# Performance work log

Hardware: AMD Instinct MI355X
Metric: run time of the kernel (lower is better)

The kernel has to match this reference:

```python
import jax, jax.numpy as jnp
import numpy as np

PSEUDO3D = True
DO_TUBE = True
DILATION_ITERATIONS = 1

# Neighbor offsets P2..P9 (clockwise from north), as in Zhang-Suen / skimage skeletonize
_OFFS = [(-1, 0), (-1, 1), (0, 1), (1, 1), (1, 0), (1, -1), (0, -1), (-1, -1)]


def _shift(a, dy, dx):
    # out[n, y, x] = a[n, y+dy, x+dx], zero-padded borders (same as skimage's 0-pad)
    N, H, W = a.shape
    p = jnp.pad(a, ((0, 0), (1, 1), (1, 1)))
    return p[:, 1 + dy:1 + dy + H, 1 + dx:1 + dx + W]


def _subiter(img, first):
    # One Zhang-Suen sub-iteration on a stack of 2D slices [N, H, W] (bool)
    P = [_shift(img, dy, dx) for dy, dx in _OFFS]
    B = sum(p.astype(jnp.int32) for p in P)            # nonzero-neighbor count
    seq = P + [P[0]]
    A = sum(((~seq[k]) & seq[k + 1]).astype(jnp.int32) for k in range(8))  # 0->1 transitions
    P2, P3, P4, P5, P6, P7, P8, P9 = P
    if first:
        c = (~(P2 & P4 & P6)) & (~(P4 & P6 & P8))
    else:
        c = (~(P2 & P4 & P8)) & (~(P2 & P6 & P8))
    remove = img & (B >= 2) & (B <= 6) & (A == 1) & c
    return img & ~remove


def _thin_stack(stack):
    # Zhang-Suen thinning of every 2D slice in a [N, H, W] bool stack, run to convergence.
    # All slices are processed in one while_loop; converged slices are fixed points, so
    # extra iterations are no-ops and the result matches per-slice skeletonize.
    def body(state):
        img, _ = state
        new = _subiter(_subiter(img, True), False)
        return new, jnp.any(new != img)

    def cond(state):
        return state[1]

    img, _ = jax.lax.while_loop(cond, body, (stack, jnp.array(True)))
    return img


def _dilate6(v):
    # scipy.ndimage.binary_dilation with the default 6-connected 3D structure, border 0
    D, H, W = v.shape
    p = jnp.pad(v, 1)
    out = v
    for dz, dy, dx in [(1, 0, 0), (-1, 0, 0), (0, 1, 0), (0, -1, 0), (0, 0, 1), (0, 0, -1)]:
        out = out | p[1 + dz:1 + dz + D, 1 + dy:1 + dy + H, 1 + dx:1 + dx + W]
    return out


def setup_inputs() -> dict:
    key = jax.random.key(0)
    gt = jax.random.randint(key, (1, 48, 384, 384), 0, 2).astype(jnp.float32)
    return {"gt_skel": gt}


def reference(gt_skel):
    vol = gt_skel[0]                      # squeeze(axis=0) -> [D, H, W]
    mask = vol == 1.0                     # bool
    skel = _thin_stack(mask)              # per z-slice skeletonize
    if PSEUDO3D:
        # per y-slice: mask[:, y, :] has shape [D, W]
        skel = skel | jnp.transpose(_thin_stack(jnp.transpose(mask, (1, 0, 2))), (1, 0, 2))
        # per x-slice: mask[:, :, x] has shape [D, H]
        skel = skel | jnp.transpose(_thin_stack(jnp.transpose(mask, (2, 0, 1))), (1, 2, 0))
    if DO_TUBE:
        for _ in range(DILATION_ITERATIONS):
            skel = _dilate6(skel)
    skel = skel & mask                    # skel &= gt_skel.astype(bool) (values are 0/1)
    return skel[None].astype(jnp.float32)
```

## Files before the change

### kernel.cpp

```cpp
#include <hip/hip_runtime.h>

typedef unsigned long long u64;

constexpr int D = 48, H = 384, W = 384;
constexpr int WPR = 6;
constexpr int PADW = 8;
constexpr int NVOX = D * H * W;
constexpr int NWVOL = D * H * WPR;
constexpr int MPAD2 = 52;

__device__ __forceinline__ void fa(u64 a, u64 b, u64 c, u64& s, u64& cy) {
  u64 x = a ^ b;
  s = x ^ c;
  cy = (a & b) | (c & x);
}

__device__ __forceinline__ u64 zs_regs(u64 w00, u64 w01, u64 w02,
                                       u64 w10, u64 w11, u64 w12,
                                       u64 w20, u64 w21, u64 w22, bool first) {
  const u64 P2 = w01;
  const u64 P3 = (w01 >> 1) | (w02 << 63);
  const u64 P4 = (w11 >> 1) | (w12 << 63);
  const u64 P5 = (w21 >> 1) | (w22 << 63);
  const u64 P6 = w21;
  const u64 P7 = (w21 << 1) | (w20 >> 63);
  const u64 P8 = (w11 << 1) | (w10 >> 63);
  const u64 P9 = (w01 << 1) | (w00 >> 63);

  u64 s1, c1, s2, c2, s3, c3, u0, u1, v1, v2;
  fa(P2, P3, P4, s1, c1);
  fa(P5, P6, P7, s2, c2);
  fa(P8, P9, 0ull, s3, c3);
  fa(s1, s2, s3, u0, u1);
  fa(c1, c2, c3, v1, v2);
  u64 b1 = u1 ^ v1, k2 = u1 & v1;
  u64 b2 = v2 ^ k2, b3 = v2 & k2;
  u64 condB = (b1 | b2 | b3) & ~(b3 | (b2 & b1 & u0));

  u64 t0 = ~P2 & P3, t1 = ~P3 & P4, t2 = ~P4 & P5, t3 = ~P5 & P6;
  u64 t4 = ~P6 & P7, t5 = ~P7 & P8, t6 = ~P8 & P9, t7 = ~P9 & P2;
  fa(t0, t1, t2, s1, c1);
  fa(t3, t4, t5, s2, c2);
  fa(t6, t7, 0ull, s3, c3);
  fa(s1, s2, s3, u0, u1);
  fa(c1, c2, c3, v1, v2);
  u64 a1 = u1 ^ v1, j2 = u1 & v1;
  u64 a2 = v2 ^ j2, a3 = v2 & j2;
  u64 condA = u0 & ~(a1 | a2 | a3);

  u64 cc = first ? ((~(P2 & P4 & P6)) & (~(P4 & P6 & P8)))
                 : ((~(P2 & P4 & P8)) & (~(P2 & P6 & P8)));
  return w11 & ~(condB & condA & cc);
}

__device__ __forceinline__ bool dirty3(const u64* U, int q) {
  const int pb = q + 64;
  const int w = pb >> 6, sh = pb & 63;
  u64 v = U[w] >> sh;
  if (sh > 61) v |= U[w + 1] << (64 - sh);
  return (v & 7ull) != 0;
}

template<int R, bool FIRST>
__device__ __forceinline__ void subpass(const u64* __restrict__ src, u64* __restrict__ dst,
                                        u64* rawW, const u64* rawPrev,
                                        u64* Uw, const u64* Ur,
                                        int* chgflag, int tid, int nthr) {
  constexpr int NP = (R + 2) * PADW;
  int anych = 0;
  for (int base = 0; base < NP; base += nthr) {
    const int idx = base + tid;
    int changed = 0;
    if (idx < NP) {
      const bool dirty = dirty3(Ur, idx - PADW - 1)
                       | dirty3(Ur, idx - 1)
                       | dirty3(Ur, idx + PADW - 1);
      if (dirty) {
        const u64 old = src[idx];
        u64 nw = 0;
        if (old) {
          const u64 n00 = src[idx - PADW - 1];
          const u64 n01 = src[idx - PADW];
          const u64 n02 = src[idx - PADW + 1];
          const u64 n10 = src[idx - 1];
          const u64 n12 = src[idx + 1];
          const u64 n20 = src[idx + PADW - 1];
          const u64 n21 = src[idx + PADW];
          const u64 n22 = src[idx + PADW + 1];
          nw = zs_regs(n00, n01, n02, n10, old, n12, n20, n21, n22, FIRST);
          changed = (nw != old);
        }
        dst[idx] = nw;
        anych |= changed;
      }
    }
    const u64 bal = __ballot(changed != 0);
    if ((tid & 63) == 0 && idx < NP) {
      const int mw = 1 + (idx >> 6);
      rawW[mw] = bal;
      Uw[mw] = bal | rawPrev[mw];
    }
  }
  if (anych) *chgflag = 1;
}

template<int R, int MODE>
__device__ __forceinline__ void thin_body(const u64* __restrict__ maskP,
                                          u64* __restrict__ skelZY,
                                          u64* __restrict__ skelX,
                                          int slice, u64* Abuf, u64* Bbuf,
                                          u64 (*raw)[MPAD2], u64 (*Um)[MPAD2],
                                          int* s_chg) {
  constexpr int NP = (R + 2) * PADW;
  constexpr int MW = (NP + 63) >> 6;
  const int tid = threadIdx.x;
  const int nthr = blockDim.x;

  if (MODE == 0 || MODE == 1) {
    for (int idx = tid; idx < NP; idx += nthr) {
      const int rp = idx >> 3, cp = idx & 7;
      u64 v = 0;
      if (rp >= 1 && rp <= R && cp >= 1 && cp <= 6) {
        if (MODE == 0) v = maskP[(slice * H + (rp - 1)) * WPR + (cp - 1)];
        else           v = maskP[((rp - 1) * H + slice) * WPR + (cp - 1)];
      }
      Abuf[idx] = v;
      Bbuf[idx] = 0;
    }
  } else {
    const int lane = tid & 63, wave = tid >> 6, nwv = nthr >> 6;
    const int xw = slice >> 6, xb = slice & 63;
    for (int w = wave; w < NP; w += nwv) {
      const int rp = w >> 3, cp = w & 7;
      u64 val = 0;
      if (rp >= 1 && rp <= R && cp >= 1 && cp <= 6) {
        const int c = (cp - 1) * 64 + lane;
        u64 bit = (maskP[((rp - 1) * H + c) * WPR + xw] >> xb) & 1ull;
        val = __ballot(bit != 0);
      }
      if (lane == 0) { Abuf[w] = val; Bbuf[w] = 0; }
    }
  }

  for (int t = tid; t < 4 * MPAD2; t += nthr) {
    const int arr = t / MPAD2, j = t - arr * MPAD2;
    const u64 v = ((arr & 1) && j >= 1 && j <= MW) ? ~0ull : 0ull;
    if (arr < 2) raw[arr][j] = v; else Um[arr - 2][j] = v;
  }
  if (tid < 2) s_chg[tid] = 0;
  __syncthreads();

  int k = 0;
  while (true) {
    subpass<R, true >(Abuf, Bbuf, raw[0], raw[1], Um[0], Um[1], &s_chg[k], tid, nthr);
    __syncthreads();
    if (tid == 0) s_chg[k ^ 1] = 0;
    subpass<R, false>(Bbuf, Abuf, raw[1], raw[0], Um[1], Um[0], &s_chg[k], tid, nthr);
    __syncthreads();
    if (s_chg[k] == 0) break;
    k ^= 1;
  }

  for (int idx = tid; idx < NP; idx += nthr) {
    const int rp = idx >> 3, cp = idx & 7;
    if (rp < 1 || rp > R || cp < 1 || cp > 6) continue;
    const u64 w = Abuf[idx];
    if (!w) continue;
    const int r = rp - 1, wc = cp - 1;
    if (MODE == 0)      atomicOr(&skelZY[(slice * H + r) * WPR + wc], w);
    else if (MODE == 1) atomicOr(&skelZY[(r * H + slice) * WPR + wc], w);
    else                skelX[(r * W + slice) * WPR + wc] = w;
  }
}

__global__ __launch_bounds__(1024) void thin_all(const u64* __restrict__ maskP,
                                                 u64* __restrict__ skelZY,
                                                 u64* __restrict__ skelX) {
  __shared__ u64 Abuf[(H + 2) * PADW];
  __shared__ u64 Bbuf[(H + 2) * PADW];
  __shared__ u64 raw[2][MPAD2];
  __shared__ u64 Um[2][MPAD2];
  __shared__ int s_chg[2];
  const int b = blockIdx.x;
  if (b < D) {
    thin_body<H, 0>(maskP, skelZY, skelX, b, Abuf, Bbuf, raw, Um, s_chg);
  } else if (b < D + H) {
    thin_body<D, 1>(maskP, skelZY, skelX, b - D, Abuf, Bbuf, raw, Um, s_chg);
  } else {
    thin_body<D, 2>(maskP, skelZY, skelX, b - D - H, Abuf, Bbuf, raw, Um, s_chg);
  }
}

__global__ void init_pack(const float* __restrict__ in, u64* __restrict__ maskP,
                          u64* __restrict__ skelZY, u64* __restrict__ skelX) {
  const int lane = threadIdx.x & 63;
  const int gwave = (blockIdx.x * blockDim.x + threadIdx.x) >> 6;
  const int nwaves = (gridDim.x * blockDim.x) >> 6;
  for (int widx = gwave; widx < NWVOL; widx += nwaves) {
    float v = in[(size_t)widx * 64 + lane];
    u64 w = __ballot(v == 1.0f);
    if (lane == 0) {
      maskP[widx] = w;
      skelZY[widx] = 0;
      skelX[widx] = 0;
    }
  }
}

__global__ void transpose_or(const u64* __restrict__ skelX,
                             u64* __restrict__ skelZY) {
  const int gw = (blockIdx.x * blockDim.x + threadIdx.x) >> 6;
  const int lane = threadIdx.x & 63;
  const int z = gw / 36, rem = gw - z * 36;
  const int yw = rem / 6, xw = rem - yw * 6;
  const int x = xw * 64 + lane;
  const u64 wx = skelX[(z * W + x) * WPR + yw];
  u64 mine = 0;
  #pragma unroll 8
  for (int j = 0; j < 64; ++j) {
    u64 wj = __ballot((wx >> j) & 1ull);
    if (lane == j) mine = wj;
  }
  const int y = yw * 64 + lane;
  if (mine) skelZY[(z * H + y) * WPR + xw] |= mine;
}

__global__ __launch_bounds__(256) void dilate_expand(const u64* __restrict__ maskP,
                                                     const u64* __restrict__ skelZY,
                                                     float* __restrict__ out) {
  __shared__ u64 rw[64];
  const int tid = threadIdx.x;
  const int wbase = blockIdx.x * 64;
  if (tid < 64) {
    const int wi = wbase + tid;
    const int wc = wi % WPR;
    const int row = wi / WPR;
    const int y = row % H;
    const int z = row / H;
    const u64 S = skelZY[wi];
    const u64 L = (wc > 0) ? skelZY[wi - 1] : 0ull;
    const u64 Rw = (wc < WPR - 1) ? skelZY[wi + 1] : 0ull;
    u64 d = S | (S << 1) | (L >> 63) | (S >> 1) | (Rw << 63);
    if (y > 0)     d |= skelZY[wi - WPR];
    if (y < H - 1) d |= skelZY[wi + WPR];
    if (z > 0)     d |= skelZY[wi - H * WPR];
    if (z < D - 1) d |= skelZY[wi + H * WPR];
    rw[tid] = d & maskP[wi];
  }
  __syncthreads();
  float4* o4 = reinterpret_cast<float4*>(out + (size_t)wbase * 64);
  #pragma unroll
  for (int k = 0; k < 4; ++k) {
    const int f = tid + 256 * k;
    const u64 bits = rw[f >> 4] >> ((f & 15) * 4);
    float4 o;
    o.x = (float)(bits & 1ull);
    o.y = (float)((bits >> 1) & 1ull);
    o.z = (float)((bits >> 2) & 1ull);
    o.w = (float)((bits >> 3) & 1ull);
    o4[f] = o;
  }
}

extern "C" void kernel_launch(void* const* d_in, const int* in_sizes, int n_in,
                              void* d_out, int out_size, void* d_ws, size_t ws_size,
                              hipStream_t stream) {
  const float* in = (const float*)d_in[0];
  float* out = (float*)d_out;
  u64* wsw = (u64*)d_ws;
  u64* maskP = wsw;
  u64* skelZY = wsw + NWVOL;
  u64* skelX = wsw + 2 * NWVOL;

  init_pack<<<1728, 256, 0, stream>>>(in, maskP, skelZY, skelX);
  thin_all<<<D + H + W, 1024, 0, stream>>>(maskP, skelZY, skelX);
  transpose_or<<<(NWVOL + 255) / 256, 256, 0, stream>>>(skelX, skelZY);
  dilate_expand<<<NWVOL / 64, 256, 0, stream>>>(maskP, skelZY, out);
}
```

Baseline: 70.70 us.

## Split z-slice thinning into haloed band pre-pass, then finish per full slice

The 48 long z-slice thinning blocks (384 rows each) were the critical path in a single launch. They are now split into 4 bands per slice with 24-row halos, each run for a fixed number of Zhang-Suen iterations alongside the x/y-slice blocks. A second kernel then finishes convergence on the full slices starting from that partial result, and fuses the x-skeleton transpose-OR using atomics. This adds redundant halo work, one more workspace buffer, and relies on the band result being a valid intermediate state so the finish pass converges to the same skeleton.

```diff
diff --git a/kernel.cpp b/kernel.cpp
--- a/kernel.cpp
+++ b/kernel.cpp
@@ -8,6 +8,13 @@
 constexpr int NVOX = D * H * W;
 constexpr int NWVOL = D * H * WPR;
 constexpr int MPAD2 = 52;
+
+constexpr int BAND = 96;
+constexpr int HALO = 24;
+constexpr int KA = 24;
+constexpr int BROWS = BAND + 2 * HALO;
+constexpr int NBAND = H / BAND;
+constexpr int NTILE = D * 36;
 
 __device__ __forceinline__ void fa(u64 a, u64 b, u64 c, u64& s, u64& cy) {
   u64 x = a ^ b;
@@ -79,15 +86,9 @@
         const u64 old = src[idx];
         u64 nw = 0;
         if (old) {
-          const u64 n00 = src[idx - PADW - 1];
-          const u64 n01 = src[idx - PADW];
-          const u64 n02 = src[idx - PADW + 1];
-          const u64 n10 = src[idx - 1];
-          const u64 n12 = src[idx + 1];
-          const u64 n20 = src[idx + PADW - 1];
-          const u64 n21 = src[idx + PADW];
-          const u64 n22 = src[idx + PADW + 1];
-          nw = zs_regs(n00, n01, n02, n10, old, n12, n20, n21, n22, FIRST);
+          nw = zs_regs(src[idx - PADW - 1], src[idx - PADW], src[idx - PADW + 1],
+                       src[idx - 1], old, src[idx + 1],
+                       src[idx + PADW - 1], src[idx + PADW], src[idx + PADW + 1], FIRST);
           changed = (nw != old);
         }
         dst[idx] = nw;
@@ -104,8 +105,17 @@
   if (anych) *chgflag = 1;
 }
 
+__device__ __forceinline__ void init_masks(u64 (*raw)[MPAD2], u64 (*Um)[MPAD2],
+                                           int MW, int tid, int nthr) {
+  for (int t = tid; t < 4 * MPAD2; t += nthr) {
+    const int arr = t / MPAD2, j = t - arr * MPAD2;
+    const u64 v = ((arr & 1) && j >= 1 && j <= MW) ? ~0ull : 0ull;
+    if (arr < 2) raw[arr][j] = v; else Um[arr - 2][j] = v;
+  }
+}
+
 template<int R, int MODE>
-__device__ __forceinline__ void thin_body(const u64* __restrict__ maskP,
+__device__ __forceinline__ void thin_body(const u64* __restrict__ src0,
                                           u64* __restrict__ skelZY,
                                           u64* __restrict__ skelX,
                                           int slice, u64* Abuf, u64* Bbuf,
@@ -121,8 +131,8 @@
       const int rp = idx >> 3, cp = idx & 7;
       u64 v = 0;
       if (rp >= 1 && rp <= R && cp >= 1 && cp <= 6) {
-        if (MODE == 0) v = maskP[(slice * H + (rp - 1)) * WPR + (cp - 1)];
-        else           v = maskP[((rp - 1) * H + slice) * WPR + (cp - 1)];
+        if (MODE == 0) v = src0[(slice * H + (rp - 1)) * WPR + (cp - 1)];
+        else           v = src0[((rp - 1) * H + slice) * WPR + (cp - 1)];
       }
       Abuf[idx] = v;
       Bbuf[idx] = 0;
@@ -135,18 +145,14 @@
       u64 val = 0;
       if (rp >= 1 && rp <= R && cp >= 1 && cp <= 6) {
         const int c = (cp - 1) * 64 + lane;
-        u64 bit = (maskP[((rp - 1) * H + c) * WPR + xw] >> xb) & 1ull;
+        u64 bit = (src0[((rp - 1) * H + c) * WPR + xw] >> xb) & 1ull;
         val = __ballot(bit != 0);
       }
       if (lane == 0) { Abuf[w] = val; Bbuf[w] = 0; }
     }
   }
 
-  for (int t = tid; t < 4 * MPAD2; t += nthr) {
-    const int arr = t / MPAD2, j = t - arr * MPAD2;
-    const u64 v = ((arr & 1) && j >= 1 && j <= MW) ? ~0ull : 0ull;
-    if (arr < 2) raw[arr][j] = v; else Um[arr - 2][j] = v;
-  }
+  init_masks(raw, Um, MW, tid, nthr);
   if (tid < 2) s_chg[tid] = 0;
   __syncthreads();
 
@@ -173,9 +179,69 @@
   }
 }
 
-__global__ __launch_bounds__(1024) void thin_all(const u64* __restrict__ maskP,
-                                                 u64* __restrict__ skelZY,
-                                                 u64* __restrict__ skelX) {
+__device__ __forceinline__ void band_body(const u64* __restrict__ maskP,
+                                          u64* __restrict__ curZ,
+                                          int zi, int band,
+                                          u64* Abuf, u64* Bbuf,
+                                          u64 (*raw)[MPAD2], u64 (*Um)[MPAD2],
+                                          int* s_chg) {
+  constexpr int NP = (BROWS + 2) * PADW;
+  constexpr int MW = (NP + 63) >> 6;
+  const int tid = threadIdx.x;
+  const int nthr = blockDim.x;
+  const int g0 = band * BAND - HALO;
+
+  for (int idx = tid; idx < NP; idx += nthr) {
+    const int rp = idx >> 3, cp = idx & 7;
+    const int g = g0 + rp - 1;
+    u64 v = 0;
+    if (rp >= 1 && rp <= BROWS && cp >= 1 && cp <= 6 && g >= 0 && g < H)
+      v = maskP[(zi * H + g) * WPR + (cp - 1)];
+    Abuf[idx] = v;
+    Bbuf[idx] = 0;
+  }
+  init_masks(raw, Um, MW, tid, nthr);
+  if (tid == 0) s_chg[0] = 0;
+  __syncthreads();
+
+  for (int t = 0; t < KA; t += 2) {
+    subpass<BROWS, true >(Abuf, Bbuf, raw[0], raw[1], Um[0], Um[1], &s_chg[0], tid, nthr);
+    __syncthreads();
+    subpass<BROWS, false>(Bbuf, Abuf, raw[1], raw[0], Um[1], Um[0], &s_chg[0], tid, nthr);
+    __syncthreads();
+  }
+
+  for (int idx = tid; idx < NP; idx += nthr) {
+    const int rp = idx >> 3, cp = idx & 7;
+    if (rp < 1 || rp > BROWS || cp < 1 || cp > 6) continue;
+    const int g = g0 + rp - 1;
+    if (g < band * BAND || g >= band * BAND + BAND) continue;
+    curZ[(zi * H + g) * WPR + (cp - 1)] = Abuf[idx];
+  }
+}
+
+__global__ __launch_bounds__(1024) void thin_bands_xy(const u64* __restrict__ maskP,
+                                                      u64* __restrict__ skelZY,
+                                                      u64* __restrict__ skelX,
+                                                      u64* __restrict__ curZ) {
+  __shared__ u64 Abuf[(BROWS + 2) * PADW];
+  __shared__ u64 Bbuf[(BROWS + 2) * PADW];
+  __shared__ u64 raw[2][MPAD2];
+  __shared__ u64 Um[2][MPAD2];
+  __shared__ int s_chg[2];
+  const int b = blockIdx.x;
+  if (b < D * NBAND) {
+    band_body(maskP, curZ, b >> 2, b & 3, Abuf, Bbuf, raw, Um, s_chg);
+  } else if (b < D * NBAND + W) {
+    thin_body<D, 2>(maskP, skelZY, skelX, b - D * NBAND, Abuf, Bbuf, raw, Um, s_chg);
+  } else {
+    thin_body<D, 1>(maskP, skelZY, skelX, b - D * NBAND - W, Abuf, Bbuf, raw, Um, s_chg);
+  }
+}
+
+__global__ __launch_bounds__(1024) void thin_z_finish(const u64* __restrict__ curZ,
+                                                      u64* __restrict__ skelZY,
+                                                      const u64* __restrict__ skelX) {
   __shared__ u64 Abuf[(H + 2) * PADW];
   __shared__ u64 Bbuf[(H + 2) * PADW];
   __shared__ u64 raw[2][MPAD2];
@@ -183,11 +249,24 @@
   __shared__ int s_chg[2];
   const int b = blockIdx.x;
   if (b < D) {
-    thin_body<H, 0>(maskP, skelZY, skelX, b, Abuf, Bbuf, raw, Um, s_chg);
-  } else if (b < D + H) {
-    thin_body<D, 1>(maskP, skelZY, skelX, b - D, Abuf, Bbuf, raw, Um, s_chg);
+    thin_body<H, 0>(curZ, skelZY, nullptr, b, Abuf, Bbuf, raw, Um, s_chg);
   } else {
-    thin_body<D, 2>(maskP, skelZY, skelX, b - D - H, Abuf, Bbuf, raw, Um, s_chg);
+    const int gw = (b - D) * 16 + (threadIdx.x >> 6);
+    if (gw < NTILE) {
+      const int lane = threadIdx.x & 63;
+      const int z = gw / 36, rem = gw - z * 36;
+      const int yw = rem / 6, xw = rem - yw * 6;
+      const int x = xw * 64 + lane;
+      const u64 wx = skelX[(z * W + x) * WPR + yw];
+      u64 mine = 0;
+      #pragma unroll 8
+      for (int j = 0; j < 64; ++j) {
+        u64 wj = __ballot((wx >> j) & 1ull);
+        if (lane == j) mine = wj;
+      }
+      const int y = yw * 64 + lane;
+      if (mine) atomicOr(&skelZY[(z * H + y) * WPR + xw], mine);
+    }
   }
 }
 
@@ -205,24 +284,6 @@
       skelX[widx] = 0;
     }
   }
-}
-
-__global__ void transpose_or(const u64* __restrict__ skelX,
-                             u64* __restrict__ skelZY) {
-  const int gw = (blockIdx.x * blockDim.x + threadIdx.x) >> 6;
-  const int lane = threadIdx.x & 63;
-  const int z = gw / 36, rem = gw - z * 36;
-  const int yw = rem / 6, xw = rem - yw * 6;
-  const int x = xw * 64 + lane;
-  const u64 wx = skelX[(z * W + x) * WPR + yw];
-  u64 mine = 0;
-  #pragma unroll 8
-  for (int j = 0; j < 64; ++j) {
-    u64 wj = __ballot((wx >> j) & 1ull);
-    if (lane == j) mine = wj;
-  }
-  const int y = yw * 64 + lane;
-  if (mine) skelZY[(z * H + y) * WPR + xw] |= mine;
 }
 
 __global__ __launch_bounds__(256) void dilate_expand(const u64* __restrict__ maskP,
@@ -271,9 +332,10 @@
   u64* maskP = wsw;
   u64* skelZY = wsw + NWVOL;
   u64* skelX = wsw + 2 * NWVOL;
+  u64* curZ = wsw + 3 * NWVOL;
 
   init_pack<<<1728, 256, 0, stream>>>(in, maskP, skelZY, skelX);
-  thin_all<<<D + H + W, 1024, 0, stream>>>(maskP, skelZY, skelX);
-  transpose_or<<<(NWVOL + 255) / 256, 256, 0, stream>>>(skelX, skelZY);
+  thin_bands_xy<<<D * NBAND + W + H, 1024, 0, stream>>>(maskP, skelZY, skelX, curZ);
+  thin_z_finish<<<D + (NTILE + 15) / 16, 1024, 0, stream>>>(curZ, skelZY, skelX);
   dilate_expand<<<NWVOL / 64, 256, 0, stream>>>(maskP, skelZY, out);
 }
```

Result: slower. 81.70 us (+15.6%).

## Thin small D-slices per wavefront and pre-transpose mask for x-slices

Applied to the files above, without the earlier changes.

The small 48-row y- and x-slice thinning problems are remapped so that each wavefront owns one slice, sixteen per block, and iterates with wave barriers instead of block-wide syncs and dirty tracking. A new transpose_in kernel builds an x-major bit mask up front, so x-slices load whole words instead of gathering bits with ballots. The large z-slices gain a coarse per-word dirty map that skips stencil work in clean regions. The cost is an extra transpose kernel, extra workspace, and full recomputation of every word on each pass in the per-wave path.

```diff
diff --git a/kernel.cpp b/kernel.cpp
--- a/kernel.cpp
+++ b/kernel.cpp
@@ -1,6 +1,7 @@
 #include <hip/hip_runtime.h>
 
 typedef unsigned long long u64;
+typedef unsigned int u32;
 
 constexpr int D = 48, H = 384, W = 384;
 constexpr int WPR = 6;
@@ -8,6 +9,11 @@
 constexpr int NVOX = D * H * W;
 constexpr int NWVOL = D * H * WPR;
 constexpr int MPAD2 = 52;
+constexpr int NPZ = (H + 2) * PADW;
+constexpr int MWZ = (NPZ + 63) >> 6;
+constexpr int NXY = (D + 2) * PADW;
+constexpr int NTILE = D * 36;
+constexpr size_t THIN_SMEM = (size_t)16 * 2 * NXY * 8;
 
 __device__ __forceinline__ void fa(u64 a, u64 b, u64 c, u64& s, u64& cy) {
   u64 x = a ^ b;
@@ -61,138 +67,172 @@
   return (v & 7ull) != 0;
 }
 
-template<int R, bool FIRST>
-__device__ __forceinline__ void subpass(const u64* __restrict__ src, u64* __restrict__ dst,
-                                        u64* rawW, const u64* rawPrev,
-                                        u64* Uw, const u64* Ur,
-                                        int* chgflag, int tid, int nthr) {
-  constexpr int NP = (R + 2) * PADW;
+template<bool FIRST>
+__device__ __forceinline__ void subpassZ(const u64* __restrict__ src, u64* __restrict__ dst,
+                                         u64* rawW, const u64* rawPrev,
+                                         u64* Uw, const u64* Ur,
+                                         u32* gmW, const u32* gmR,
+                                         int* chgflag, int tid, int nthr) {
   int anych = 0;
-  for (int base = 0; base < NP; base += nthr) {
+  for (int base = 0; base < NPZ; base += nthr) {
     const int idx = base + tid;
     int changed = 0;
-    if (idx < NP) {
-      const bool dirty = dirty3(Ur, idx - PADW - 1)
-                       | dirty3(Ur, idx - 1)
-                       | dirty3(Ur, idx + PADW - 1);
-      if (dirty) {
-        const u64 old = src[idx];
-        u64 nw = 0;
-        if (old) {
-          const u64 n00 = src[idx - PADW - 1];
-          const u64 n01 = src[idx - PADW];
-          const u64 n02 = src[idx - PADW + 1];
-          const u64 n10 = src[idx - 1];
-          const u64 n12 = src[idx + 1];
-          const u64 n20 = src[idx + PADW - 1];
-          const u64 n21 = src[idx + PADW];
-          const u64 n22 = src[idx + PADW + 1];
-          nw = zs_regs(n00, n01, n02, n10, old, n12, n20, n21, n22, FIRST);
-          changed = (nw != old);
+    const bool valid = idx < NPZ;
+    if (valid) {
+      const int mw = 1 + (idx >> 6);
+      if (gmR[mw - 1] | gmR[mw] | gmR[mw + 1]) {
+        const bool dirty = dirty3(Ur, idx - PADW - 1)
+                         | dirty3(Ur, idx - 1)
+                         | dirty3(Ur, idx + PADW - 1);
+        if (dirty) {
+          const u64 old = src[idx];
+          u64 nw = 0;
+          if (old) {
+            nw = zs_regs(src[idx - PADW - 1], src[idx - PADW], src[idx - PADW + 1],
+                         src[idx - 1], old, src[idx + 1],
+                         src[idx + PADW - 1], src[idx + PADW], src[idx + PADW + 1], FIRST);
+            changed = (nw != old);
+          }
+          dst[idx] = nw;
+          anych |= changed;
         }
-        dst[idx] = nw;
-        anych |= changed;
       }
     }
     const u64 bal = __ballot(changed != 0);
-    if ((tid & 63) == 0 && idx < NP) {
+    if ((tid & 63) == 0 && valid) {
       const int mw = 1 + (idx >> 6);
       rawW[mw] = bal;
-      Uw[mw] = bal | rawPrev[mw];
+      const u64 uw = bal | rawPrev[mw];
+      Uw[mw] = uw;
+      gmW[mw] = (uw != 0ull) ? 1u : 0u;
     }
   }
   if (anych) *chgflag = 1;
 }
 
-template<int R, int MODE>
-__device__ __forceinline__ void thin_body(const u64* __restrict__ maskP,
-                                          u64* __restrict__ skelZY,
-                                          u64* __restrict__ skelX,
-                                          int slice, u64* Abuf, u64* Bbuf,
-                                          u64 (*raw)[MPAD2], u64 (*Um)[MPAD2],
-                                          int* s_chg) {
-  constexpr int NP = (R + 2) * PADW;
-  constexpr int MW = (NP + 63) >> 6;
+template<bool FIRST>
+__device__ __forceinline__ void pass_xy(volatile u64* S, volatile u64* Dd,
+                                        int lane, u64& anyc) {
+  #pragma unroll
+  for (int k = 0; k < 7; ++k) {
+    const int idx = lane + (k << 6);
+    if (idx >= NXY) break;
+    const u64 old = S[idx];
+    u64 nw = 0;
+    if (old) {
+      const u64 n00 = S[idx - 9], n01 = S[idx - 8], n02 = S[idx - 7];
+      const u64 n10 = S[idx - 1],                   n12 = S[idx + 1];
+      const u64 n20 = S[idx + 7], n21 = S[idx + 8], n22 = S[idx + 9];
+      nw = zs_regs(n00, n01, n02, n10, old, n12, n20, n21, n22, FIRST);
+    }
+    Dd[idx] = nw;
+    anyc |= (old ^ nw);
+  }
+}
+
+__global__ __launch_bounds__(1024) void thin_all(const u64* __restrict__ maskP,
+                                                 const u64* __restrict__ maskX,
+                                                 u64* __restrict__ skelZY,
+                                                 u64* __restrict__ skelX) {
+  extern __shared__ u64 smem[];
+  __shared__ int s_chg[2];
+  const int b = blockIdx.x;
   const int tid = threadIdx.x;
-  const int nthr = blockDim.x;
-
-  if (MODE == 0 || MODE == 1) {
-    for (int idx = tid; idx < NP; idx += nthr) {
+
+  if (b < D) {
+    u64* A = smem;
+    u64* B = A + NPZ;
+    u64* raw0 = B + NPZ;
+    u64* raw1 = raw0 + MPAD2;
+    u64* Um0 = raw1 + MPAD2;
+    u64* Um1 = Um0 + MPAD2;
+    u32* gm0 = (u32*)(Um1 + MPAD2);
+    u32* gm1 = gm0 + MPAD2;
+
+    for (int idx = tid; idx < NPZ; idx += 1024) {
       const int rp = idx >> 3, cp = idx & 7;
       u64 v = 0;
-      if (rp >= 1 && rp <= R && cp >= 1 && cp <= 6) {
-        if (MODE == 0) v = maskP[(slice * H + (rp - 1)) * WPR + (cp - 1)];
-        else           v = maskP[((rp - 1) * H + slice) * WPR + (cp - 1)];
+      if (rp >= 1 && rp <= H && cp >= 1 && cp <= WPR)
+        v = maskP[(b * H + (rp - 1)) * WPR + (cp - 1)];
+      A[idx] = v;
+      B[idx] = 0;
+    }
+    for (int t = tid; t < 4 * MPAD2; t += 1024) {
+      const int arr = t / MPAD2, j = t - arr * MPAD2;
+      const u64 v = ((arr & 1) && j >= 1 && j <= MWZ) ? ~0ull : 0ull;
+      if (arr == 0) raw0[j] = v;
+      else if (arr == 1) raw1[j] = v;
+      else if (arr == 2) Um0[j] = v;
+      else Um1[j] = v;
+    }
+    for (int t = tid; t < 2 * MPAD2; t += 1024) {
+      const int arr = t / MPAD2, j = t - arr * MPAD2;
+      const u32 v = (arr == 1 && j >= 1 && j <= MWZ) ? 1u : 0u;
+      if (arr == 0) gm0[j] = v; else gm1[j] = v;
+    }
+    if (tid < 2) s_chg[tid] = 0;
+    __syncthreads();
+
+    int k = 0;
+    while (true) {
+      subpassZ<true >(A, B, raw0, raw1, Um0, Um1, gm0, gm1, &s_chg[k], tid, 1024);
+      __syncthreads();
+      if (tid == 0) s_chg[k ^ 1] = 0;
+      subpassZ<false>(B, A, raw1, raw0, Um1, Um0, gm1, gm0, &s_chg[k], tid, 1024);
+      __syncthreads();
+      if (s_chg[k] == 0) break;
+      k ^= 1;
+    }
+
+    for (int idx = tid; idx < NPZ; idx += 1024) {
+      const int rp = idx >> 3, cp = idx & 7;
+      if (rp < 1 || rp > H || cp < 1 || cp > WPR) continue;
+      const u64 w = A[idx];
+      if (!w) continue;
+      atomicOr(&skelZY[(b * H + (rp - 1)) * WPR + (cp - 1)], w);
+    }
+  } else {
+    const int wave = tid >> 6, lane = tid & 63;
+    const int s = (b - D) * 16 + wave;
+    volatile u64* A = smem + wave * (2 * NXY);
+    volatile u64* Bv = A + NXY;
+
+    for (int idx = lane; idx < NXY; idx += 64) {
+      const int rp = idx >> 3, cp = idx & 7;
+      u64 v = 0;
+      if (rp >= 1 && rp <= D && cp >= 1 && cp <= WPR) {
+        if (s < W) v = maskX[((rp - 1) * W + s) * WPR + (cp - 1)];
+        else       v = maskP[((rp - 1) * H + (s - W)) * WPR + (cp - 1)];
       }
-      Abuf[idx] = v;
-      Bbuf[idx] = 0;
-    }
-  } else {
-    const int lane = tid & 63, wave = tid >> 6, nwv = nthr >> 6;
-    const int xw = slice >> 6, xb = slice & 63;
-    for (int w = wave; w < NP; w += nwv) {
-      const int rp = w >> 3, cp = w & 7;
-      u64 val = 0;
-      if (rp >= 1 && rp <= R && cp >= 1 && cp <= 6) {
-        const int c = (cp - 1) * 64 + lane;
-        u64 bit = (maskP[((rp - 1) * H + c) * WPR + xw] >> xb) & 1ull;
-        val = __ballot(bit != 0);
+      A[idx] = v;
+      Bv[idx] = 0;
+    }
+    __builtin_amdgcn_wave_barrier();
+
+    while (true) {
+      u64 anyc = 0;
+      pass_xy<true >(A, Bv, lane, anyc);
+      __builtin_amdgcn_wave_barrier();
+      pass_xy<false>(Bv, A, lane, anyc);
+      __builtin_amdgcn_wave_barrier();
+      if (__ballot(anyc != 0) == 0) break;
+    }
+
+    for (int idx = lane; idx < NXY; idx += 64) {
+      const int rp = idx >> 3, cp = idx & 7;
+      if (rp < 1 || rp > D || cp < 1 || cp > WPR) continue;
+      const u64 w = A[idx];
+      if (s < W) {
+        skelX[((rp - 1) * W + s) * WPR + (cp - 1)] = w;
+      } else if (w) {
+        atomicOr(&skelZY[((rp - 1) * H + (s - W)) * WPR + (cp - 1)], w);
       }
-      if (lane == 0) { Abuf[w] = val; Bbuf[w] = 0; }
-    }
-  }
-
-  for (int t = tid; t < 4 * MPAD2; t += nthr) {
-    const int arr = t / MPAD2, j = t - arr * MPAD2;
-    const u64 v = ((arr & 1) && j >= 1 && j <= MW) ? ~0ull : 0ull;
-    if (arr < 2) raw[arr][j] = v; else Um[arr - 2][j] = v;
-  }
-  if (tid < 2) s_chg[tid] = 0;
-  __syncthreads();
-
-  int k = 0;
-  while (true) {
-    subpass<R, true >(Abuf, Bbuf, raw[0], raw[1], Um[0], Um[1], &s_chg[k], tid, nthr);
-    __syncthreads();
-    if (tid == 0) s_chg[k ^ 1] = 0;
-    subpass<R, false>(Bbuf, Abuf, raw[1], raw[0], Um[1], Um[0], &s_chg[k], tid, nthr);
-    __syncthreads();
-    if (s_chg[k] == 0) break;
-    k ^= 1;
-  }
-
-  for (int idx = tid; idx < NP; idx += nthr) {
-    const int rp = idx >> 3, cp = idx & 7;
-    if (rp < 1 || rp > R || cp < 1 || cp > 6) continue;
-    const u64 w = Abuf[idx];
-    if (!w) continue;
-    const int r = rp - 1, wc = cp - 1;
-    if (MODE == 0)      atomicOr(&skelZY[(slice * H + r) * WPR + wc], w);
-    else if (MODE == 1) atomicOr(&skelZY[(r * H + slice) * WPR + wc], w);
-    else                skelX[(r * W + slice) * WPR + wc] = w;
-  }
-}
-
-__global__ __launch_bounds__(1024) void thin_all(const u64* __restrict__ maskP,
-                                                 u64* __restrict__ skelZY,
-                                                 u64* __restrict__ skelX) {
-  __shared__ u64 Abuf[(H + 2) * PADW];
-  __shared__ u64 Bbuf[(H + 2) * PADW];
-  __shared__ u64 raw[2][MPAD2];
-  __shared__ u64 Um[2][MPAD2];
-  __shared__ int s_chg[2];
-  const int b = blockIdx.x;
-  if (b < D) {
-    thin_body<H, 0>(maskP, skelZY, skelX, b, Abuf, Bbuf, raw, Um, s_chg);
-  } else if (b < D + H) {
-    thin_body<D, 1>(maskP, skelZY, skelX, b - D, Abuf, Bbuf, raw, Um, s_chg);
-  } else {
-    thin_body<D, 2>(maskP, skelZY, skelX, b - D - H, Abuf, Bbuf, raw, Um, s_chg);
+    }
   }
 }
 
 __global__ void init_pack(const float* __restrict__ in, u64* __restrict__ maskP,
-                          u64* __restrict__ skelZY, u64* __restrict__ skelX) {
+                          u64* __restrict__ skelZY) {
   const int lane = threadIdx.x & 63;
   const int gwave = (blockIdx.x * blockDim.x + threadIdx.x) >> 6;
   const int nwaves = (gridDim.x * blockDim.x) >> 6;
@@ -202,9 +242,23 @@
     if (lane == 0) {
       maskP[widx] = w;
       skelZY[widx] = 0;
-      skelX[widx] = 0;
-    }
-  }
+    }
+  }
+}
+
+__global__ void transpose_in(const u64* __restrict__ maskP, u64* __restrict__ maskX) {
+  const int gw = (blockIdx.x * blockDim.x + threadIdx.x) >> 6;
+  const int lane = threadIdx.x & 63;
+  const int z = gw / 36, rem = gw - z * 36;
+  const int yw = rem / 6, xw = rem - yw * 6;
+  const u64 wp = maskP[(z * H + yw * 64 + lane) * WPR + xw];
+  u64 mine = 0;
+  #pragma unroll 8
+  for (int i = 0; i < 64; ++i) {
+    u64 wi = __ballot((wp >> i) & 1ull);
+    if (lane == i) mine = wi;
+  }
+  maskX[(z * W + xw * 64 + lane) * WPR + yw] = mine;
 }
 
 __global__ void transpose_or(const u64* __restrict__ skelX,
@@ -271,9 +325,15 @@
   u64* maskP = wsw;
   u64* skelZY = wsw + NWVOL;
   u64* skelX = wsw + 2 * NWVOL;
-
-  init_pack<<<1728, 256, 0, stream>>>(in, maskP, skelZY, skelX);
-  thin_all<<<D + H + W, 1024, 0, stream>>>(maskP, skelZY, skelX);
+  u64* maskX = wsw + 3 * NWVOL;
+
+  (void)hipFuncSetAttribute((const void*)thin_all,
+                            hipFuncAttributeMaxDynamicSharedMemorySize,
+                            (int)THIN_SMEM);
+
+  init_pack<<<1728, 256, 0, stream>>>(in, maskP, skelZY);
+  transpose_in<<<(NTILE * 64) / 256, 256, 0, stream>>>(maskP, maskX);
+  thin_all<<<D + 768 / 16, 1024, THIN_SMEM, stream>>>(maskP, maskX, skelZY, skelX);
   transpose_or<<<(NWVOL + 255) / 256, 256, 0, stream>>>(skelX, skelZY);
   dilate_expand<<<NWVOL / 64, 256, 0, stream>>>(maskP, skelZY, out);
 }
```

Measured after the change: 220.6 us. +212.0%, slower.
